# Kernel tuning notes

Measured on AMD Instinct MI355X. Metric: run time of the kernel, lower is better.

## Reference

```python
import jax, jax.numpy as jnp
import numpy as np

N_NODES = 100000
N_EDGES = 1600000
DIMS = [100, 200, 128, 128]
EPS = 1e-5


def setup_inputs() -> dict:
    key = jax.random.key(0)
    ks = jax.random.split(key, 32)
    inp = {
        "x": jax.random.normal(ks[0], (N_NODES, DIMS[0]), dtype=jnp.float32),
        "edge_row": jnp.sort(jax.random.randint(ks[1], (N_EDGES,), 0, N_NODES, dtype=jnp.int32)),
        "edge_col": jax.random.randint(ks[2], (N_EDGES,), 0, N_NODES, dtype=jnp.int32),
        "edge_val": jax.random.uniform(ks[3], (N_EDGES,), dtype=jnp.float32),
    }
    # GCwithself layer params: neighbor-agg linear W,b and self linear Ws,bs
    ki = 4
    for i in range(3):
        fi, fo = DIMS[i], DIMS[i + 1]
        s = 1.0 / np.sqrt(fi)
        inp[f"gc{i}_W"] = jax.random.uniform(ks[ki], (fi, fo), minval=-s, maxval=s); ki += 1
        inp[f"gc{i}_b"] = jnp.zeros((fo,), jnp.float32)
        inp[f"gc{i}_Ws"] = jax.random.uniform(ks[ki], (fi, fo), minval=-s, maxval=s); ki += 1
        inp[f"gc{i}_bs"] = jnp.zeros((fo,), jnp.float32)
    s = 1.0 / np.sqrt(128)
    inp["fc1_W"] = jax.random.uniform(ks[ki], (128, 128), minval=-s, maxval=s); ki += 1
    inp["fc1_b"] = jnp.zeros((128,), jnp.float32)
    inp["fc2a_W"] = jax.random.uniform(ks[ki], (128, 256), minval=-s, maxval=s); ki += 1
    inp["fc2a_b"] = jnp.zeros((256,), jnp.float32)
    inp["bn_g"] = jnp.ones((256,), jnp.float32)
    inp["bn_b"] = jnp.zeros((256,), jnp.float32)
    s2 = 1.0 / np.sqrt(256)
    inp["fc2b_W"] = jax.random.uniform(ks[ki], (256, 18), minval=-s2, maxval=s2); ki += 1
    inp["fc2b_b"] = jnp.zeros((18,), jnp.float32)
    return inp


def _gc_layer(x, row, col, val, W, b, Ws, bs):
    # spmm: (adj @ x) via gather + segment-sum, then linear + self-linear + ReLU
    agg = jax.ops.segment_sum(val[:, None] * x[col], row, num_segments=N_NODES)
    return jax.nn.relu(agg @ W + b + x @ Ws + bs)


def _batchnorm(h, g, b):
    mu = jnp.mean(h, axis=0)
    var = jnp.var(h, axis=0)
    return (h - mu) * jax.lax.rsqrt(var + EPS) * g + b


def reference(x, edge_row, edge_col, edge_val,
              gc0_W, gc0_b, gc0_Ws, gc0_bs,
              gc1_W, gc1_b, gc1_Ws, gc1_bs,
              gc2_W, gc2_b, gc2_Ws, gc2_bs,
              fc1_W, fc1_b, fc2a_W, fc2a_b, bn_g, bn_b, fc2b_W, fc2b_b):
    h = _gc_layer(x, edge_row, edge_col, edge_val, gc0_W, gc0_b, gc0_Ws, gc0_bs)
    h = _gc_layer(h, edge_row, edge_col, edge_val, gc1_W, gc1_b, gc1_Ws, gc1_bs)
    h = _gc_layer(h, edge_row, edge_col, edge_val, gc2_W, gc2_b, gc2_Ws, gc2_bs)
    h = jax.nn.relu(h @ fc1_W + fc1_b)
    h = _batchnorm(h @ fc2a_W + fc2a_b, bn_g, bn_b)
    h = jax.nn.relu(h)
    return h @ fc2b_W + fc2b_b
```

## Files before the change

kernel.cpp:

```cpp
#include <hip/hip_runtime.h>

#define N_NODES 100000
#define N_EDGES 1600000

typedef __attribute__((ext_vector_type(8))) short bf16x8;
typedef __attribute__((ext_vector_type(4))) float f32x4;

__device__ __forceinline__ unsigned short f2bf(float f) {
    unsigned u = __float_as_uint(f);
    u = (u + 0x7FFFu + ((u >> 16) & 1u)) >> 16;
    return (unsigned short)u;
}
__device__ __forceinline__ float bf2f(unsigned short h) {
    return __uint_as_float(((unsigned)h) << 16);
}
__device__ __forceinline__ float bflo(unsigned w) { return __uint_as_float(w << 16); }
__device__ __forceinline__ float bfhi(unsigned w) { return __uint_as_float(w & 0xFFFF0000u); }

__global__ void build_row_ptr(const int* __restrict__ row, int* __restrict__ rp) {
    int n = blockIdx.x * blockDim.x + threadIdx.x;
    if (n > N_NODES) return;
    int lo = 0, hi = N_EDGES;
    while (lo < hi) {
        int mid = (lo + hi) >> 1;
        if (row[mid] < n) lo = mid + 1; else hi = mid;
    }
    rp[n] = lo;
}

__global__ __launch_bounds__(256) void conv_x(const float* __restrict__ x,
                                              unsigned short* __restrict__ xb) {
    const int total = N_NODES * 104;
    for (int i = blockIdx.x * 256 + threadIdx.x; i < total; i += gridDim.x * 256) {
        int r = i / 104, c = i - r * 104;
        xb[i] = (c < 100) ? f2bf(x[(size_t)r * 100 + c]) : (unsigned short)0;
    }
}

__global__ __launch_bounds__(256) void prep_all(
    const float* __restrict__ gc0W, const float* __restrict__ gc0Ws,
    const float* __restrict__ gc1W, const float* __restrict__ gc1Ws,
    const float* __restrict__ gc2W, const float* __restrict__ gc2Ws,
    const float* __restrict__ f1W,  const float* __restrict__ f2aW,
    const float* __restrict__ f2bW,
    const float* __restrict__ gc0b, const float* __restrict__ gc0bs,
    const float* __restrict__ gc2b, const float* __restrict__ gc2bs,
    const float* __restrict__ gc1b, const float* __restrict__ gc1bs,
    unsigned short* __restrict__ Bt0, unsigned short* __restrict__ Bt1,
    unsigned short* __restrict__ Bt2, unsigned short* __restrict__ Btf1,
    unsigned short* __restrict__ Btf2a, unsigned short* __restrict__ Btf2b,
    float* __restrict__ bias0, float* __restrict__ bias2, float* __restrict__ bias1)
{
    int i = blockIdx.x * 256 + threadIdx.x;
    if (i < 44800) {
        int n = i / 224, k = i - n * 224; float v = 0.f;
        if (k < 104) { if (k < 100) v = gc0W[(size_t)k * 200 + n]; }
        else { int kr = k - 104; if (kr < 100) v = gc0Ws[(size_t)kr * 200 + n]; }
        Bt0[i] = f2bf(v); return;
    }
    i -= 44800;
    if (i < 57344) {
        int n = i / 224, k = i - n * 224; float v = 0.f;
        if (k < 200) v = (n < 128) ? gc1W[(size_t)k * 128 + n] : gc1Ws[(size_t)k * 128 + (n - 128)];
        Bt1[i] = f2bf(v); return;
    }
    i -= 57344;
    if (i < 32768) {
        int n = i / 256, k = i - n * 256; float v;
        if (k < 128) v = gc2W[(size_t)k * 128 + n];
        else         v = gc2Ws[(size_t)(k - 128) * 128 + n];
        Bt2[i] = f2bf(v); return;
    }
    i -= 32768;
    if (i < 16384) { int n = i >> 7, k = i & 127; Btf1[i] = f2bf(f1W[(size_t)k * 128 + n]); return; }
    i -= 16384;
    if (i < 32768) { int n = i >> 7, k = i & 127; Btf2a[i] = f2bf(f2aW[(size_t)k * 256 + n]); return; }
    i -= 32768;
    if (i < 4608) { int n = i >> 8, k = i & 255; Btf2b[i] = f2bf(f2bW[(size_t)k * 18 + n]); return; }
    i -= 4608;
    if (i < 200) { bias0[i] = gc0b[i] + gc0bs[i]; return; }
    i -= 200;
    if (i < 128) { bias2[i] = gc2b[i] + gc2bs[i]; return; }
    i -= 128;
    if (i < 128) { bias1[i] = gc1b[i] + gc1bs[i]; return; }
}

template<int FUSE>
__global__ __launch_bounds__(256) void spmm_v4(
    const unsigned short* __restrict__ xin, int ldin, int F,
    const int* __restrict__ rp, const int* __restrict__ col,
    const float* __restrict__ val, const float* __restrict__ b01,
    unsigned short* __restrict__ outp, int ldout)
{
    const int node = blockIdx.x * 16 + (threadIdx.x >> 4);
    const int l16 = threadIdx.x & 15;
    const int f8 = l16 * 8;
    const bool act = f8 < F;
    const int e0 = rp[node], e1 = rp[node + 1];
    const unsigned short* xf = xin + f8;

    float a[8];
#pragma unroll
    for (int k = 0; k < 8; k++) a[k] = 0.f;

    for (int e = e0; e < e1; e += 4) {
        int   cj[4]; float vj[4];
#pragma unroll
        for (int j = 0; j < 4; j++) {
            int ej = e + j;
            bool m = ej < e1;
            int es = m ? ej : e0;
            cj[j] = col[es];
            float vv = val[es];
            vj[j] = m ? vv : 0.f;
        }
        if (act) {
#pragma unroll
            for (int j = 0; j < 4; j++) {
                uint4 u = *(const uint4*)(xf + (size_t)cj[j] * ldin);
                float v = vj[j];
                a[0] += v * bflo(u.x); a[1] += v * bfhi(u.x);
                a[2] += v * bflo(u.y); a[3] += v * bfhi(u.y);
                a[4] += v * bflo(u.z); a[5] += v * bfhi(u.z);
                a[6] += v * bflo(u.w); a[7] += v * bfhi(u.w);
            }
        }
    }

    if (act) {
        if (FUSE) {
            uint4 uz = *(const uint4*)(xin + (size_t)node * ldin + 128 + f8);
            float z[8] = {bflo(uz.x), bfhi(uz.x), bflo(uz.y), bfhi(uz.y),
                          bflo(uz.z), bfhi(uz.z), bflo(uz.w), bfhi(uz.w)};
#pragma unroll
            for (int k = 0; k < 8; k++)
                a[k] = fmaxf(a[k] + z[k] + b01[f8 + k], 0.f);
        }
        uint4 pk;
        pk.x = ((unsigned)f2bf(a[1]) << 16) | (unsigned)f2bf(a[0]);
        pk.y = ((unsigned)f2bf(a[3]) << 16) | (unsigned)f2bf(a[2]);
        pk.z = ((unsigned)f2bf(a[5]) << 16) | (unsigned)f2bf(a[4]);
        pk.w = ((unsigned)f2bf(a[7]) << 16) | (unsigned)f2bf(a[6]);
        *(uint4*)(outp + (size_t)node * ldout + f8) = pk;
    }
}

__global__ __launch_bounds__(256, 2) void gemm_head(
    const unsigned short* __restrict__ agg0, const unsigned short* __restrict__ xb,
    const unsigned short* __restrict__ Bt0, const float* __restrict__ bias0,
    const unsigned short* __restrict__ Bt1,
    unsigned short* __restrict__ yz, int M)
{
    __shared__ __align__(16) unsigned short As[64][40];
    __shared__ __align__(16) unsigned short Bs[256][40];
    __shared__ __align__(16) unsigned short H[64][232];

    const int tid = threadIdx.x;
    const int rowBase = blockIdx.x * 64;
    const int wave = tid >> 6, lane = tid & 63;
    const int wc = wave * 64;
    const int lrow = lane & 15, lq = lane >> 4;

    {
        f32x4 acc[4][4] = {};
        for (int kk = 0; kk < 224; kk += 32) {
            {
                int row = tid >> 2;
                int kof = (tid & 3) * 8;
                int k0 = kk + kof;
                uint4 av = make_uint4(0, 0, 0, 0);
                int gr = rowBase + row;
                if (gr < M && k0 < 208) {
                    av = (k0 < 104) ? *(const uint4*)(agg0 + (size_t)gr * 104 + k0)
                                    : *(const uint4*)(xb   + (size_t)gr * 104 + (k0 - 104));
                }
                *(uint4*)&As[row][kof] = av;
            }
#pragma unroll
            for (int i = 0; i < 4; ++i) {
                int c = tid + 256 * i;
                int row = c >> 2;
                int kof = (c & 3) * 8;
                uint4 bv = make_uint4(0, 0, 0, 0);
                if (row < 200) bv = *(const uint4*)(Bt0 + (size_t)row * 224 + kk + kof);
                *(uint4*)&Bs[row][kof] = bv;
            }
            __syncthreads();
            bf16x8 af[4], bfr[4];
#pragma unroll
            for (int m = 0; m < 4; ++m) af[m] = *(const bf16x8*)&As[16 * m + lrow][lq * 8];
#pragma unroll
            for (int n = 0; n < 4; ++n) bfr[n] = *(const bf16x8*)&Bs[wc + 16 * n + lrow][lq * 8];
#pragma unroll
            for (int m = 0; m < 4; ++m)
#pragma unroll
                for (int n = 0; n < 4; ++n)
                    acc[m][n] = __builtin_amdgcn_mfma_f32_16x16x32_bf16(af[m], bfr[n], acc[m][n], 0, 0, 0);
            __syncthreads();
        }
#pragma unroll
        for (int n = 0; n < 4; ++n) {
            int colg = wc + 16 * n + lrow;
            if (colg >= 224) continue;
            float bb = (colg < 200) ? bias0[colg] : 0.f;
#pragma unroll
            for (int m = 0; m < 4; ++m)
#pragma unroll
                for (int r = 0; r < 4; ++r) {
                    int rowl = 16 * m + lq * 4 + r;
                    H[rowl][colg] = f2bf(fmaxf(acc[m][n][r] + bb, 0.f));
                }
        }
    }
    __syncthreads();

    {
        f32x4 acc[4][4] = {};
        for (int kk = 0; kk < 224; kk += 32) {
#pragma unroll
            for (int i = 0; i < 4; ++i) {
                int c = tid + 256 * i;
                int row = c >> 2;
                int kof = (c & 3) * 8;
                *(uint4*)&Bs[row][kof] = *(const uint4*)(Bt1 + (size_t)row * 224 + kk + kof);
            }
            __syncthreads();
            bf16x8 af[4], bfr[4];
#pragma unroll
            for (int m = 0; m < 4; ++m) af[m] = *(const bf16x8*)&H[16 * m + lrow][kk + lq * 8];
#pragma unroll
            for (int n = 0; n < 4; ++n) bfr[n] = *(const bf16x8*)&Bs[wc + 16 * n + lrow][lq * 8];
#pragma unroll
            for (int m = 0; m < 4; ++m)
#pragma unroll
                for (int n = 0; n < 4; ++n)
                    acc[m][n] = __builtin_amdgcn_mfma_f32_16x16x32_bf16(af[m], bfr[n], acc[m][n], 0, 0, 0);
            __syncthreads();
        }
#pragma unroll
        for (int n = 0; n < 4; ++n) {
            int colg = wc + 16 * n + lrow;
#pragma unroll
            for (int m = 0; m < 4; ++m)
#pragma unroll
                for (int r = 0; r < 4; ++r) {
                    int rowg = rowBase + 16 * m + lq * 4 + r;
                    if (rowg < M)
                        yz[(size_t)rowg * 256 + colg] = f2bf(acc[m][n][r]);
                }
        }
    }
}

template<int OUTBF, int APPLYBN>
__global__ __launch_bounds__(256) void gemm_mfma(
    const unsigned short* __restrict__ A0, const unsigned short* __restrict__ A1,
    int lda0, int lda1, int K0, int Ktot,
    const unsigned short* __restrict__ Bt, int ldk,
    const float* __restrict__ bias, void* __restrict__ Cv,
    int M, int N, int ldc, int relu, const float* __restrict__ stats)
{
    __shared__ __align__(16) unsigned short As[128][56];
    __shared__ __align__(16) unsigned short Bs[128][56];

    const int tid = threadIdx.x;
    const int rowBase = blockIdx.y * 128;
    const int colBase = blockIdx.x * 128;
    const int wave = tid >> 6, lane = tid & 63;
    const int wr = (wave >> 1) * 64, wc = (wave & 1) * 64;
    const int lrow = lane & 15, lq = lane >> 4;

    f32x4 acc[4][4] = {};

    for (int kk = 0; kk < ldk; kk += 32) {
#pragma unroll
        for (int i = 0; i < 2; ++i) {
            int c = tid + 256 * i;
            int row = c >> 2;
            int kof = (c & 3) * 8;
            int k0 = kk + kof;
            uint4 av = make_uint4(0, 0, 0, 0);
            int gr = rowBase + row;
            if (gr < M && k0 < Ktot) {
                const unsigned short* src; int krel;
                if (k0 < K0) { src = A0 + (size_t)gr * lda0; krel = k0; }
                else         { src = A1 + (size_t)gr * lda1; krel = k0 - K0; }
                av = *(const uint4*)(src + krel);
                if (APPLYBN) {
                    const float* sc = stats + 512 + k0;
                    const float* sh = stats + 768 + k0;
                    unsigned r[4] = {av.x, av.y, av.z, av.w};
#pragma unroll
                    for (int j = 0; j < 4; j++) {
                        float lo = bflo(r[j]) * sc[2 * j] + sh[2 * j];
                        float hi = bfhi(r[j]) * sc[2 * j + 1] + sh[2 * j + 1];
                        lo = fmaxf(lo, 0.f); hi = fmaxf(hi, 0.f);
                        r[j] = ((unsigned)f2bf(hi) << 16) | (unsigned)f2bf(lo);
                    }
                    av = make_uint4(r[0], r[1], r[2], r[3]);
                }
            }
            *(uint4*)&As[row][kof] = av;
            uint4 bv = make_uint4(0, 0, 0, 0);
            int n0 = colBase + row;
            if (n0 < N) bv = *(const uint4*)(Bt + (size_t)n0 * ldk + kk + kof);
            *(uint4*)&Bs[row][kof] = bv;
        }
        __syncthreads();

        bf16x8 af[4], bfr[4];
#pragma unroll
        for (int m = 0; m < 4; ++m) af[m] = *(const bf16x8*)&As[wr + 16 * m + lrow][lq * 8];
#pragma unroll
        for (int n = 0; n < 4; ++n) bfr[n] = *(const bf16x8*)&Bs[wc + 16 * n + lrow][lq * 8];
#pragma unroll
        for (int m = 0; m < 4; ++m)
#pragma unroll
            for (int n = 0; n < 4; ++n)
                acc[m][n] = __builtin_amdgcn_mfma_f32_16x16x32_bf16(af[m], bfr[n], acc[m][n], 0, 0, 0);
        __syncthreads();
    }

#pragma unroll
    for (int m = 0; m < 4; ++m) {
#pragma unroll
        for (int n = 0; n < 4; ++n) {
            int colg = colBase + wc + 16 * n + lrow;
            if (colg >= N) continue;
            float bb = bias ? bias[colg] : 0.f;
#pragma unroll
            for (int r = 0; r < 4; ++r) {
                int rowg = rowBase + wr + 16 * m + lq * 4 + r;
                if (rowg >= M) continue;
                float v = acc[m][n][r] + bb;
                if (relu) v = fmaxf(v, 0.f);
                if (OUTBF) ((unsigned short*)Cv)[(size_t)rowg * ldc + colg] = f2bf(v);
                else       ((float*)Cv)[(size_t)rowg * ldc + colg] = v;
            }
        }
    }
}

__global__ __launch_bounds__(256, 2) void gemm_tail(
    const unsigned short* __restrict__ agg2, const unsigned short* __restrict__ h1,
    const unsigned short* __restrict__ Bt2, const float* __restrict__ bias2,
    const unsigned short* __restrict__ Btf1, const float* __restrict__ fc1b,
    const unsigned short* __restrict__ Btf2a, const float* __restrict__ fc2ab,
    unsigned short* __restrict__ h4, float* __restrict__ stats, int M)
{
    __shared__ __align__(16) unsigned short As[128][56];
    __shared__ __align__(16) unsigned short Bs[256][56];
    __shared__ __align__(16) unsigned short H23[128][136];
    __shared__ float sred[512];

    const int tid = threadIdx.x;
    const int rowBase = blockIdx.x * 128;
    const int wave = tid >> 6, lane = tid & 63;
    const int wr = (wave >> 1) * 64, wc = (wave & 1) * 64;
    const int lrow = lane & 15, lq = lane >> 4;

    {
        f32x4 acc[4][4] = {};
        for (int kk = 0; kk < 256; kk += 32) {
#pragma unroll
            for (int i = 0; i < 2; ++i) {
                int c = tid + 256 * i;
                int row = c >> 2;
                int kof = (c & 3) * 8;
                int k0 = kk + kof;
                uint4 av = make_uint4(0, 0, 0, 0);
                int gr = rowBase + row;
                if (gr < M) {
                    av = (k0 < 128) ? *(const uint4*)(agg2 + (size_t)gr * 128 + k0)
                                    : *(const uint4*)(h1   + (size_t)gr * 128 + (k0 - 128));
                }
                *(uint4*)&As[row][kof] = av;
                *(uint4*)&Bs[row][kof] = *(const uint4*)(Bt2 + (size_t)row * 256 + k0);
            }
            __syncthreads();
            bf16x8 af[4], bfr[4];
#pragma unroll
            for (int m = 0; m < 4; ++m) af[m] = *(const bf16x8*)&As[wr + 16 * m + lrow][lq * 8];
#pragma unroll
            for (int n = 0; n < 4; ++n) bfr[n] = *(const bf16x8*)&Bs[wc + 16 * n + lrow][lq * 8];
#pragma unroll
            for (int m = 0; m < 4; ++m)
#pragma unroll
                for (int n = 0; n < 4; ++n)
                    acc[m][n] = __builtin_amdgcn_mfma_f32_16x16x32_bf16(af[m], bfr[n], acc[m][n], 0, 0, 0);
            __syncthreads();
        }
#pragma unroll
        for (int n = 0; n < 4; ++n) {
            int colg = wc + 16 * n + lrow;
            float bb = bias2[colg];
#pragma unroll
            for (int m = 0; m < 4; ++m)
#pragma unroll
                for (int r = 0; r < 4; ++r) {
                    int rowl = wr + 16 * m + lq * 4 + r;
                    H23[rowl][colg] = f2bf(fmaxf(acc[m][n][r] + bb, 0.f));
                }
        }
    }
    __syncthreads();

    {
        f32x4 acc[4][4] = {};
        for (int kk = 0; kk < 128; kk += 32) {
#pragma unroll
            for (int i = 0; i < 2; ++i) {
                int c = tid + 256 * i;
                int row = c >> 2;
                int kof = (c & 3) * 8;
                *(uint4*)&Bs[row][kof] = *(const uint4*)(Btf1 + (size_t)row * 128 + kk + kof);
            }
            __syncthreads();
            bf16x8 af[4], bfr[4];
#pragma unroll
            for (int m = 0; m < 4; ++m) af[m] = *(const bf16x8*)&H23[wr + 16 * m + lrow][kk + lq * 8];
#pragma unroll
            for (int n = 0; n < 4; ++n) bfr[n] = *(const bf16x8*)&Bs[wc + 16 * n + lrow][lq * 8];
#pragma unroll
            for (int m = 0; m < 4; ++m)
#pragma unroll
                for (int n = 0; n < 4; ++n)
                    acc[m][n] = __builtin_amdgcn_mfma_f32_16x16x32_bf16(af[m], bfr[n], acc[m][n], 0, 0, 0);
            __syncthreads();
        }
#pragma unroll
        for (int n = 0; n < 4; ++n) {
            int colg = wc + 16 * n + lrow;
            float bb = fc1b[colg];
#pragma unroll
            for (int m = 0; m < 4; ++m)
#pragma unroll
                for (int r = 0; r < 4; ++r) {
                    int rowl = wr + 16 * m + lq * 4 + r;
                    H23[rowl][colg] = f2bf(fmaxf(acc[m][n][r] + bb, 0.f));
                }
        }
    }
    __syncthreads();

    {
        f32x4 acc[4][8] = {};
        for (int kk = 0; kk < 128; kk += 32) {
#pragma unroll
            for (int i = 0; i < 4; ++i) {
                int c = tid + 256 * i;
                int row = c >> 2;
                int kof = (c & 3) * 8;
                *(uint4*)&Bs[row][kof] = *(const uint4*)(Btf2a + (size_t)row * 128 + kk + kof);
            }
            __syncthreads();
            bf16x8 af[4], bfr[8];
#pragma unroll
            for (int m = 0; m < 4; ++m) af[m] = *(const bf16x8*)&H23[wr + 16 * m + lrow][kk + lq * 8];
#pragma unroll
            for (int nh = 0; nh < 2; ++nh)
#pragma unroll
                for (int nm = 0; nm < 4; ++nm)
                    bfr[nh * 4 + nm] = *(const bf16x8*)&Bs[128 * nh + wc + 16 * nm + lrow][lq * 8];
#pragma unroll
            for (int m = 0; m < 4; ++m)
#pragma unroll
                for (int n = 0; n < 8; ++n)
                    acc[m][n] = __builtin_amdgcn_mfma_f32_16x16x32_bf16(af[m], bfr[n], acc[m][n], 0, 0, 0);
            __syncthreads();
        }

        for (int j = tid; j < 512; j += 256) sred[j] = 0.f;
        __syncthreads();
#pragma unroll
        for (int nh = 0; nh < 2; ++nh)
#pragma unroll
            for (int nm = 0; nm < 4; ++nm) {
                int colg = 128 * nh + wc + 16 * nm + lrow;
                float bb = fc2ab[colg];
                float s = 0.f, s2 = 0.f;
#pragma unroll
                for (int m = 0; m < 4; ++m)
#pragma unroll
                    for (int r = 0; r < 4; ++r) {
                        int rowg = rowBase + wr + 16 * m + lq * 4 + r;
                        if (rowg < M) {
                            float v = acc[m][nh * 4 + nm][r] + bb;
                            h4[(size_t)rowg * 256 + colg] = f2bf(v);
                            s += v; s2 += v * v;
                        }
                    }
                atomicAdd(&sred[colg], s);
                atomicAdd(&sred[256 + colg], s2);
            }
        __syncthreads();
        for (int j = tid; j < 512; j += 256) atomicAdd(&stats[j], sred[j]);
    }
}

__global__ void bn_finalize(float* __restrict__ stats,
                            const float* __restrict__ g,
                            const float* __restrict__ b) {
    int t = threadIdx.x;
    const float invN = 1.f / (float)N_NODES;
    float mu = stats[t] * invN;
    float var = stats[256 + t] * invN - mu * mu;
    float sc = g[t] * rsqrtf(var + 1e-5f);
    stats[512 + t] = sc;
    stats[768 + t] = b[t] - mu * sc;
}

extern "C" void kernel_launch(void* const* d_in, const int* in_sizes, int n_in,
                              void* d_out, int out_size, void* d_ws, size_t ws_size,
                              hipStream_t stream) {
    const float* x        = (const float*)d_in[0];
    const int*   edge_row = (const int*)  d_in[1];
    const int*   edge_col = (const int*)  d_in[2];
    const float* edge_val = (const float*)d_in[3];
    const float* gc0_W  = (const float*)d_in[4];
    const float* gc0_b  = (const float*)d_in[5];
    const float* gc0_Ws = (const float*)d_in[6];
    const float* gc0_bs = (const float*)d_in[7];
    const float* gc1_W  = (const float*)d_in[8];
    const float* gc1_b  = (const float*)d_in[9];
    const float* gc1_Ws = (const float*)d_in[10];
    const float* gc1_bs = (const float*)d_in[11];
    const float* gc2_W  = (const float*)d_in[12];
    const float* gc2_b  = (const float*)d_in[13];
    const float* gc2_Ws = (const float*)d_in[14];
    const float* gc2_bs = (const float*)d_in[15];
    const float* fc1_W  = (const float*)d_in[16];
    const float* fc1_b  = (const float*)d_in[17];
    const float* fc2a_W = (const float*)d_in[18];
    const float* fc2a_b = (const float*)d_in[19];
    const float* bn_g   = (const float*)d_in[20];
    const float* bn_b   = (const float*)d_in[21];
    const float* fc2b_W = (const float*)d_in[22];
    const float* fc2b_b = (const float*)d_in[23];
    float* out = (float*)d_out;

    char* ws = (char*)d_ws;
    int*   rowptr = (int*)ws;
    float* stats  = (float*)(ws + 512 * 1024);
    size_t o = 520 * 1024;
    unsigned short* Bt0   = (unsigned short*)(ws + o); o += 200 * 224 * 2;
    unsigned short* Bt1   = (unsigned short*)(ws + o); o += 256 * 224 * 2;
    unsigned short* Bt2   = (unsigned short*)(ws + o); o += 128 * 256 * 2;
    unsigned short* Btf1  = (unsigned short*)(ws + o); o += 128 * 128 * 2;
    unsigned short* Btf2a = (unsigned short*)(ws + o); o += 256 * 128 * 2;
    unsigned short* Btf2b = (unsigned short*)(ws + o); o += 18 * 256 * 2;
    float* bias0 = (float*)(ws + o); o += 200 * 4;
    float* bias2 = (float*)(ws + o); o += 128 * 4;
    float* bias1 = (float*)(ws + o); o += 128 * 4;
    const size_t SLOT = 52u * 1024 * 1024;
    char* S1 = ws + 1 * 1024 * 1024;
    char* S2 = S1 + SLOT;
    char* S3 = S2 + SLOT;

    unsigned short* xb   = (unsigned short*)S1;
    unsigned short* agg0 = (unsigned short*)S2;
    unsigned short* yz   = (unsigned short*)S3;
    unsigned short* h1   = (unsigned short*)S1;
    unsigned short* agg2 = (unsigned short*)S2;
    unsigned short* h4   = (unsigned short*)S3;

    build_row_ptr<<<392, 256, 0, stream>>>(edge_row, rowptr);
    conv_x<<<2048, 256, 0, stream>>>(x, xb);
    prep_all<<<(189128 + 255) / 256, 256, 0, stream>>>(
        gc0_W, gc0_Ws, gc1_W, gc1_Ws, gc2_W, gc2_Ws, fc1_W, fc2a_W, fc2b_W,
        gc0_b, gc0_bs, gc2_b, gc2_bs, gc1_b, gc1_bs,
        Bt0, Bt1, Bt2, Btf1, Btf2a, Btf2b, bias0, bias2, bias1);
    hipMemsetAsync(stats, 0, 512 * sizeof(float), stream);

    const int spmmGrid = N_NODES / 16;

    spmm_v4<0><<<spmmGrid, 256, 0, stream>>>(xb, 104, 104, rowptr, edge_col, edge_val,
                                             nullptr, agg0, 104);
    gemm_head<<<(N_NODES + 63) / 64, 256, 0, stream>>>(agg0, xb, Bt0, bias0, Bt1, yz, N_NODES);
    spmm_v4<1><<<spmmGrid, 256, 0, stream>>>(yz, 256, 128, rowptr, edge_col, edge_val,
                                             bias1, h1, 128);
    spmm_v4<0><<<spmmGrid, 256, 0, stream>>>(h1, 128, 128, rowptr, edge_col, edge_val,
                                             nullptr, agg2, 128);
    gemm_tail<<<(N_NODES + 127) / 128, 256, 0, stream>>>(
        agg2, h1, Bt2, bias2, Btf1, fc1_b, Btf2a, fc2a_b, h4, stats, N_NODES);
    bn_finalize<<<1, 256, 0, stream>>>(stats, bn_g, bn_b);
    {
        dim3 g(1, (N_NODES + 127) / 128);
        gemm_mfma<0, 1><<<g, 256, 0, stream>>>(h4, h4, 256, 256, 256, 256, Btf2b, 256,
                                               fc2b_b, out, N_NODES, 18, 18, 0, stats);
    }
}
```

Baseline: 537.9 us.

## Load MFMA fragments directly from global memory, shrink tail tiles, specialize fc2b

The dense GEMM kernels (head, tail, and final fc2b) stop staging A and B tiles through shared memory with barriers. Each lane now loads its MFMA fragments straight from global memory, and shared memory is kept only for the intermediate activations. gemm_tail moves to 64-row tiles with occupancy hint 4. The generic gemm_mfma call for the 18-column output is replaced by a dedicated kernel that gives each wave 32 rows and skips the unused columns. This removes LDS traffic and synchronization and raises occupancy, at the cost of redundant global/L2 loads of weights across waves and less coalesced fragment reads.

```diff
diff --git a/kernel.cpp b/kernel.cpp
--- a/kernel.cpp
+++ b/kernel.cpp
@@ -16,6 +16,10 @@
 }
 __device__ __forceinline__ float bflo(unsigned w) { return __uint_as_float(w << 16); }
 __device__ __forceinline__ float bfhi(unsigned w) { return __uint_as_float(w & 0xFFFF0000u); }
+
+__device__ __forceinline__ bf16x8 ld_frag(const unsigned short* p) {
+    return *(const bf16x8*)p;
+}
 
 __global__ void build_row_ptr(const int* __restrict__ row, int* __restrict__ rp) {
     int n = blockIdx.x * blockDim.x + threadIdx.x;
@@ -145,62 +149,51 @@
     }
 }
 
-__global__ __launch_bounds__(256, 2) void gemm_head(
+__global__ __launch_bounds__(256, 4) void gemm_head(
     const unsigned short* __restrict__ agg0, const unsigned short* __restrict__ xb,
     const unsigned short* __restrict__ Bt0, const float* __restrict__ bias0,
     const unsigned short* __restrict__ Bt1,
     unsigned short* __restrict__ yz, int M)
 {
-    __shared__ __align__(16) unsigned short As[64][40];
-    __shared__ __align__(16) unsigned short Bs[256][40];
     __shared__ __align__(16) unsigned short H[64][232];
 
     const int tid = threadIdx.x;
     const int rowBase = blockIdx.x * 64;
     const int wave = tid >> 6, lane = tid & 63;
-    const int wc = wave * 64;
+    const int cb = wave * 64;
     const int lrow = lane & 15, lq = lane >> 4;
+    const int kq = lq * 8;
 
     {
         f32x4 acc[4][4] = {};
         for (int kk = 0; kk < 224; kk += 32) {
-            {
-                int row = tid >> 2;
-                int kof = (tid & 3) * 8;
-                int k0 = kk + kof;
-                uint4 av = make_uint4(0, 0, 0, 0);
-                int gr = rowBase + row;
-                if (gr < M && k0 < 208) {
-                    av = (k0 < 104) ? *(const uint4*)(agg0 + (size_t)gr * 104 + k0)
-                                    : *(const uint4*)(xb   + (size_t)gr * 104 + (k0 - 104));
-                }
-                *(uint4*)&As[row][kof] = av;
+            int k0 = kk + kq;
+            bf16x8 af[4], bfr[4];
+#pragma unroll
+            for (int m = 0; m < 4; ++m) {
+                int gr = rowBase + 16 * m + lrow;
+                bf16x8 t = {};
+                if (gr < M && k0 < 208)
+                    t = (k0 < 104) ? ld_frag(agg0 + (size_t)gr * 104 + k0)
+                                   : ld_frag(xb   + (size_t)gr * 104 + (k0 - 104));
+                af[m] = t;
             }
 #pragma unroll
-            for (int i = 0; i < 4; ++i) {
-                int c = tid + 256 * i;
-                int row = c >> 2;
-                int kof = (c & 3) * 8;
-                uint4 bv = make_uint4(0, 0, 0, 0);
-                if (row < 200) bv = *(const uint4*)(Bt0 + (size_t)row * 224 + kk + kof);
-                *(uint4*)&Bs[row][kof] = bv;
+            for (int n = 0; n < 4; ++n) {
+                int nr = cb + 16 * n + lrow;
+                bf16x8 t = {};
+                if (nr < 200) t = ld_frag(Bt0 + (size_t)nr * 224 + k0);
+                bfr[n] = t;
             }
-            __syncthreads();
-            bf16x8 af[4], bfr[4];
-#pragma unroll
-            for (int m = 0; m < 4; ++m) af[m] = *(const bf16x8*)&As[16 * m + lrow][lq * 8];
-#pragma unroll
-            for (int n = 0; n < 4; ++n) bfr[n] = *(const bf16x8*)&Bs[wc + 16 * n + lrow][lq * 8];
 #pragma unroll
             for (int m = 0; m < 4; ++m)
 #pragma unroll
                 for (int n = 0; n < 4; ++n)
                     acc[m][n] = __builtin_amdgcn_mfma_f32_16x16x32_bf16(af[m], bfr[n], acc[m][n], 0, 0, 0);
-            __syncthreads();
         }
 #pragma unroll
         for (int n = 0; n < 4; ++n) {
-            int colg = wc + 16 * n + lrow;
+            int colg = cb + 16 * n + lrow;
             if (colg >= 224) continue;
             float bb = (colg < 200) ? bias0[colg] : 0.f;
 #pragma unroll
@@ -217,29 +210,22 @@
     {
         f32x4 acc[4][4] = {};
         for (int kk = 0; kk < 224; kk += 32) {
-#pragma unroll
-            for (int i = 0; i < 4; ++i) {
-                int c = tid + 256 * i;
-                int row = c >> 2;
-                int kof = (c & 3) * 8;
-                *(uint4*)&Bs[row][kof] = *(const uint4*)(Bt1 + (size_t)row * 224 + kk + kof);
-            }
-            __syncthreads();
+            int k0 = kk + kq;
             bf16x8 af[4], bfr[4];
 #pragma unroll
-            for (int m = 0; m < 4; ++m) af[m] = *(const bf16x8*)&H[16 * m + lrow][kk + lq * 8];
-#pragma unroll
-            for (int n = 0; n < 4; ++n) bfr[n] = *(const bf16x8*)&Bs[wc + 16 * n + lrow][lq * 8];
+            for (int m = 0; m < 4; ++m) af[m] = *(const bf16x8*)&H[16 * m + lrow][k0];
+#pragma unroll
+            for (int n = 0; n < 4; ++n)
+                bfr[n] = ld_frag(Bt1 + (size_t)(cb + 16 * n + lrow) * 224 + k0);
 #pragma unroll
             for (int m = 0; m < 4; ++m)
 #pragma unroll
                 for (int n = 0; n < 4; ++n)
                     acc[m][n] = __builtin_amdgcn_mfma_f32_16x16x32_bf16(af[m], bfr[n], acc[m][n], 0, 0, 0);
-            __syncthreads();
         }
 #pragma unroll
         for (int n = 0; n < 4; ++n) {
-            int colg = wc + 16 * n + lrow;
+            int colg = cb + 16 * n + lrow;
 #pragma unroll
             for (int m = 0; m < 4; ++m)
 #pragma unroll
@@ -252,247 +238,133 @@
     }
 }
 
-template<int OUTBF, int APPLYBN>
-__global__ __launch_bounds__(256) void gemm_mfma(
-    const unsigned short* __restrict__ A0, const unsigned short* __restrict__ A1,
-    int lda0, int lda1, int K0, int Ktot,
-    const unsigned short* __restrict__ Bt, int ldk,
-    const float* __restrict__ bias, void* __restrict__ Cv,
-    int M, int N, int ldc, int relu, const float* __restrict__ stats)
-{
-    __shared__ __align__(16) unsigned short As[128][56];
-    __shared__ __align__(16) unsigned short Bs[128][56];
-
-    const int tid = threadIdx.x;
-    const int rowBase = blockIdx.y * 128;
-    const int colBase = blockIdx.x * 128;
-    const int wave = tid >> 6, lane = tid & 63;
-    const int wr = (wave >> 1) * 64, wc = (wave & 1) * 64;
-    const int lrow = lane & 15, lq = lane >> 4;
-
-    f32x4 acc[4][4] = {};
-
-    for (int kk = 0; kk < ldk; kk += 32) {
-#pragma unroll
-        for (int i = 0; i < 2; ++i) {
-            int c = tid + 256 * i;
-            int row = c >> 2;
-            int kof = (c & 3) * 8;
-            int k0 = kk + kof;
-            uint4 av = make_uint4(0, 0, 0, 0);
-            int gr = rowBase + row;
-            if (gr < M && k0 < Ktot) {
-                const unsigned short* src; int krel;
-                if (k0 < K0) { src = A0 + (size_t)gr * lda0; krel = k0; }
-                else         { src = A1 + (size_t)gr * lda1; krel = k0 - K0; }
-                av = *(const uint4*)(src + krel);
-                if (APPLYBN) {
-                    const float* sc = stats + 512 + k0;
-                    const float* sh = stats + 768 + k0;
-                    unsigned r[4] = {av.x, av.y, av.z, av.w};
-#pragma unroll
-                    for (int j = 0; j < 4; j++) {
-                        float lo = bflo(r[j]) * sc[2 * j] + sh[2 * j];
-                        float hi = bfhi(r[j]) * sc[2 * j + 1] + sh[2 * j + 1];
-                        lo = fmaxf(lo, 0.f); hi = fmaxf(hi, 0.f);
-                        r[j] = ((unsigned)f2bf(hi) << 16) | (unsigned)f2bf(lo);
-                    }
-                    av = make_uint4(r[0], r[1], r[2], r[3]);
-                }
-            }
-            *(uint4*)&As[row][kof] = av;
-            uint4 bv = make_uint4(0, 0, 0, 0);
-            int n0 = colBase + row;
-            if (n0 < N) bv = *(const uint4*)(Bt + (size_t)n0 * ldk + kk + kof);
-            *(uint4*)&Bs[row][kof] = bv;
-        }
-        __syncthreads();
-
-        bf16x8 af[4], bfr[4];
-#pragma unroll
-        for (int m = 0; m < 4; ++m) af[m] = *(const bf16x8*)&As[wr + 16 * m + lrow][lq * 8];
-#pragma unroll
-        for (int n = 0; n < 4; ++n) bfr[n] = *(const bf16x8*)&Bs[wc + 16 * n + lrow][lq * 8];
-#pragma unroll
-        for (int m = 0; m < 4; ++m)
-#pragma unroll
-            for (int n = 0; n < 4; ++n)
-                acc[m][n] = __builtin_amdgcn_mfma_f32_16x16x32_bf16(af[m], bfr[n], acc[m][n], 0, 0, 0);
-        __syncthreads();
-    }
-
-#pragma unroll
-    for (int m = 0; m < 4; ++m) {
-#pragma unroll
-        for (int n = 0; n < 4; ++n) {
-            int colg = colBase + wc + 16 * n + lrow;
-            if (colg >= N) continue;
-            float bb = bias ? bias[colg] : 0.f;
-#pragma unroll
-            for (int r = 0; r < 4; ++r) {
-                int rowg = rowBase + wr + 16 * m + lq * 4 + r;
-                if (rowg >= M) continue;
-                float v = acc[m][n][r] + bb;
-                if (relu) v = fmaxf(v, 0.f);
-                if (OUTBF) ((unsigned short*)Cv)[(size_t)rowg * ldc + colg] = f2bf(v);
-                else       ((float*)Cv)[(size_t)rowg * ldc + colg] = v;
-            }
-        }
-    }
-}
-
-__global__ __launch_bounds__(256, 2) void gemm_tail(
+__global__ __launch_bounds__(256, 4) void gemm_tail(
     const unsigned short* __restrict__ agg2, const unsigned short* __restrict__ h1,
     const unsigned short* __restrict__ Bt2, const float* __restrict__ bias2,
     const unsigned short* __restrict__ Btf1, const float* __restrict__ fc1b,
     const unsigned short* __restrict__ Btf2a, const float* __restrict__ fc2ab,
     unsigned short* __restrict__ h4, float* __restrict__ stats, int M)
 {
-    __shared__ __align__(16) unsigned short As[128][56];
-    __shared__ __align__(16) unsigned short Bs[256][56];
-    __shared__ __align__(16) unsigned short H23[128][136];
+    __shared__ __align__(16) unsigned short H[64][136];
     __shared__ float sred[512];
 
     const int tid = threadIdx.x;
-    const int rowBase = blockIdx.x * 128;
+    const int rowBase = blockIdx.x * 64;
     const int wave = tid >> 6, lane = tid & 63;
-    const int wr = (wave >> 1) * 64, wc = (wave & 1) * 64;
     const int lrow = lane & 15, lq = lane >> 4;
+    const int kq = lq * 8;
 
     {
+        const int cb = wave * 32;
+        f32x4 acc[4][2] = {};
+        for (int kk = 0; kk < 256; kk += 32) {
+            int k0 = kk + kq;
+            const unsigned short* Asrc = (kk < 128) ? agg2 : h1;
+            int krel = (kk < 128) ? k0 : k0 - 128;
+            bf16x8 af[4], bfr[2];
+#pragma unroll
+            for (int m = 0; m < 4; ++m) {
+                int gr = rowBase + 16 * m + lrow;
+                bf16x8 t = {};
+                if (gr < M) t = ld_frag(Asrc + (size_t)gr * 128 + krel);
+                af[m] = t;
+            }
+#pragma unroll
+            for (int n = 0; n < 2; ++n)
+                bfr[n] = ld_frag(Bt2 + (size_t)(cb + 16 * n + lrow) * 256 + k0);
+#pragma unroll
+            for (int m = 0; m < 4; ++m)
+#pragma unroll
+                for (int n = 0; n < 2; ++n)
+                    acc[m][n] = __builtin_amdgcn_mfma_f32_16x16x32_bf16(af[m], bfr[n], acc[m][n], 0, 0, 0);
+        }
+#pragma unroll
+        for (int n = 0; n < 2; ++n) {
+            int colg = cb + 16 * n + lrow;
+            float bb = bias2[colg];
+#pragma unroll
+            for (int m = 0; m < 4; ++m)
+#pragma unroll
+                for (int r = 0; r < 4; ++r) {
+                    int rowl = 16 * m + lq * 4 + r;
+                    H[rowl][colg] = f2bf(fmaxf(acc[m][n][r] + bb, 0.f));
+                }
+        }
+    }
+    __syncthreads();
+
+    {
+        const int cb = wave * 32;
+        f32x4 acc[4][2] = {};
+        for (int kk = 0; kk < 128; kk += 32) {
+            int k0 = kk + kq;
+            bf16x8 af[4], bfr[2];
+#pragma unroll
+            for (int m = 0; m < 4; ++m) af[m] = *(const bf16x8*)&H[16 * m + lrow][k0];
+#pragma unroll
+            for (int n = 0; n < 2; ++n)
+                bfr[n] = ld_frag(Btf1 + (size_t)(cb + 16 * n + lrow) * 128 + k0);
+#pragma unroll
+            for (int m = 0; m < 4; ++m)
+#pragma unroll
+                for (int n = 0; n < 2; ++n)
+                    acc[m][n] = __builtin_amdgcn_mfma_f32_16x16x32_bf16(af[m], bfr[n], acc[m][n], 0, 0, 0);
+        }
+        __syncthreads();
+#pragma unroll
+        for (int n = 0; n < 2; ++n) {
+            int colg = cb + 16 * n + lrow;
+            float bb = fc1b[colg];
+#pragma unroll
+            for (int m = 0; m < 4; ++m)
+#pragma unroll
+                for (int r = 0; r < 4; ++r) {
+                    int rowl = 16 * m + lq * 4 + r;
+                    H[rowl][colg] = f2bf(fmaxf(acc[m][n][r] + bb, 0.f));
+                }
+        }
+    }
+    __syncthreads();
+
+    {
+        const int cb = wave * 64;
         f32x4 acc[4][4] = {};
-        for (int kk = 0; kk < 256; kk += 32) {
-#pragma unroll
-            for (int i = 0; i < 2; ++i) {
-                int c = tid + 256 * i;
-                int row = c >> 2;
-                int kof = (c & 3) * 8;
-                int k0 = kk + kof;
-                uint4 av = make_uint4(0, 0, 0, 0);
-                int gr = rowBase + row;
-                if (gr < M) {
-                    av = (k0 < 128) ? *(const uint4*)(agg2 + (size_t)gr * 128 + k0)
-                                    : *(const uint4*)(h1   + (size_t)gr * 128 + (k0 - 128));
-                }
-                *(uint4*)&As[row][kof] = av;
-                *(uint4*)&Bs[row][kof] = *(const uint4*)(Bt2 + (size_t)row * 256 + k0);
-            }
-            __syncthreads();
+        for (int kk = 0; kk < 128; kk += 32) {
+            int k0 = kk + kq;
             bf16x8 af[4], bfr[4];
 #pragma unroll
-            for (int m = 0; m < 4; ++m) af[m] = *(const bf16x8*)&As[wr + 16 * m + lrow][lq * 8];
-#pragma unroll
-            for (int n = 0; n < 4; ++n) bfr[n] = *(const bf16x8*)&Bs[wc + 16 * n + lrow][lq * 8];
+            for (int m = 0; m < 4; ++m) af[m] = *(const bf16x8*)&H[16 * m + lrow][k0];
+#pragma unroll
+            for (int n = 0; n < 4; ++n)
+                bfr[n] = ld_frag(Btf2a + (size_t)(cb + 16 * n + lrow) * 128 + k0);
 #pragma unroll
             for (int m = 0; m < 4; ++m)
 #pragma unroll
                 for (int n = 0; n < 4; ++n)
                     acc[m][n] = __builtin_amdgcn_mfma_f32_16x16x32_bf16(af[m], bfr[n], acc[m][n], 0, 0, 0);
-            __syncthreads();
-        }
-#pragma unroll
-        for (int n = 0; n < 4; ++n) {
-            int colg = wc + 16 * n + lrow;
-            float bb = bias2[colg];
-#pragma unroll
-            for (int m = 0; m < 4; ++m)
-#pragma unroll
-                for (int r = 0; r < 4; ++r) {
-                    int rowl = wr + 16 * m + lq * 4 + r;
-                    H23[rowl][colg] = f2bf(fmaxf(acc[m][n][r] + bb, 0.f));
-                }
-        }
-    }
-    __syncthreads();
-
-    {
-        f32x4 acc[4][4] = {};
-        for (int kk = 0; kk < 128; kk += 32) {
-#pragma unroll
-            for (int i = 0; i < 2; ++i) {
-                int c = tid + 256 * i;
-                int row = c >> 2;
-                int kof = (c & 3) * 8;
-                *(uint4*)&Bs[row][kof] = *(const uint4*)(Btf1 + (size_t)row * 128 + kk + kof);
-            }
-            __syncthreads();
-            bf16x8 af[4], bfr[4];
-#pragma unroll
-            for (int m = 0; m < 4; ++m) af[m] = *(const bf16x8*)&H23[wr + 16 * m + lrow][kk + lq * 8];
-#pragma unroll
-            for (int n = 0; n < 4; ++n) bfr[n] = *(const bf16x8*)&Bs[wc + 16 * n + lrow][lq * 8];
-#pragma unroll
-            for (int m = 0; m < 4; ++m)
-#pragma unroll
-                for (int n = 0; n < 4; ++n)
-                    acc[m][n] = __builtin_amdgcn_mfma_f32_16x16x32_bf16(af[m], bfr[n], acc[m][n], 0, 0, 0);
-            __syncthreads();
-        }
-#pragma unroll
-        for (int n = 0; n < 4; ++n) {
-            int colg = wc + 16 * n + lrow;
-            float bb = fc1b[colg];
-#pragma unroll
-            for (int m = 0; m < 4; ++m)
-#pragma unroll
-                for (int r = 0; r < 4; ++r) {
-                    int rowl = wr + 16 * m + lq * 4 + r;
-                    H23[rowl][colg] = f2bf(fmaxf(acc[m][n][r] + bb, 0.f));
-                }
-        }
-    }
-    __syncthreads();
-
-    {
-        f32x4 acc[4][8] = {};
-        for (int kk = 0; kk < 128; kk += 32) {
-#pragma unroll
-            for (int i = 0; i < 4; ++i) {
-                int c = tid + 256 * i;
-                int row = c >> 2;
-                int kof = (c & 3) * 8;
-                *(uint4*)&Bs[row][kof] = *(const uint4*)(Btf2a + (size_t)row * 128 + kk + kof);
-            }
-            __syncthreads();
-            bf16x8 af[4], bfr[8];
-#pragma unroll
-            for (int m = 0; m < 4; ++m) af[m] = *(const bf16x8*)&H23[wr + 16 * m + lrow][kk + lq * 8];
-#pragma unroll
-            for (int nh = 0; nh < 2; ++nh)
-#pragma unroll
-                for (int nm = 0; nm < 4; ++nm)
-                    bfr[nh * 4 + nm] = *(const bf16x8*)&Bs[128 * nh + wc + 16 * nm + lrow][lq * 8];
-#pragma unroll
-            for (int m = 0; m < 4; ++m)
-#pragma unroll
-                for (int n = 0; n < 8; ++n)
-                    acc[m][n] = __builtin_amdgcn_mfma_f32_16x16x32_bf16(af[m], bfr[n], acc[m][n], 0, 0, 0);
-            __syncthreads();
         }
 
         for (int j = tid; j < 512; j += 256) sred[j] = 0.f;
         __syncthreads();
 #pragma unroll
-        for (int nh = 0; nh < 2; ++nh)
-#pragma unroll
-            for (int nm = 0; nm < 4; ++nm) {
-                int colg = 128 * nh + wc + 16 * nm + lrow;
-                float bb = fc2ab[colg];
-                float s = 0.f, s2 = 0.f;
-#pragma unroll
-                for (int m = 0; m < 4; ++m)
-#pragma unroll
-                    for (int r = 0; r < 4; ++r) {
-                        int rowg = rowBase + wr + 16 * m + lq * 4 + r;
-                        if (rowg < M) {
-                            float v = acc[m][nh * 4 + nm][r] + bb;
-                            h4[(size_t)rowg * 256 + colg] = f2bf(v);
-                            s += v; s2 += v * v;
-                        }
+        for (int n = 0; n < 4; ++n) {
+            int colg = cb + 16 * n + lrow;
+            float bb = fc2ab[colg];
+            float s = 0.f, s2 = 0.f;
+#pragma unroll
+            for (int m = 0; m < 4; ++m)
+#pragma unroll
+                for (int r = 0; r < 4; ++r) {
+                    int rowg = rowBase + 16 * m + lq * 4 + r;
+                    if (rowg < M) {
+                        float v = acc[m][n][r] + bb;
+                        h4[(size_t)rowg * 256 + colg] = f2bf(v);
+                        s += v; s2 += v * v;
                     }
-                atomicAdd(&sred[colg], s);
-                atomicAdd(&sred[256 + colg], s2);
-            }
+                }
+            atomicAdd(&sred[colg], s);
+            atomicAdd(&sred[256 + colg], s2);
+        }
         __syncthreads();
         for (int j = tid; j < 512; j += 256) atomicAdd(&stats[j], sred[j]);
     }
@@ -508,6 +380,67 @@
     float sc = g[t] * rsqrtf(var + 1e-5f);
     stats[512 + t] = sc;
     stats[768 + t] = b[t] - mu * sc;
+}
+
+__global__ __launch_bounds__(256, 4) void fc2b_kernel(
+    const unsigned short* __restrict__ h4, const unsigned short* __restrict__ Btf2b,
+    const float* __restrict__ bias, const float* __restrict__ stats,
+    float* __restrict__ out, int M)
+{
+    const int tid = threadIdx.x;
+    const int wave = tid >> 6, lane = tid & 63;
+    const int lrow = lane & 15, lq = lane >> 4;
+    const int kq = lq * 8;
+    const int rowBase = blockIdx.x * 128 + wave * 32;
+
+    f32x4 acc[2][2] = {};
+    for (int kk = 0; kk < 256; kk += 32) {
+        int k0 = kk + kq;
+        const float* sc = stats + 512 + k0;
+        const float* sh = stats + 768 + k0;
+        bf16x8 af[2], bfr[2];
+#pragma unroll
+        for (int m = 0; m < 2; ++m) {
+            int gr = rowBase + 16 * m + lrow;
+            uint4 u = make_uint4(0, 0, 0, 0);
+            if (gr < M) u = *(const uint4*)(h4 + (size_t)gr * 256 + k0);
+            unsigned w[4] = {u.x, u.y, u.z, u.w};
+#pragma unroll
+            for (int j = 0; j < 4; j++) {
+                float lo = fmaxf(bflo(w[j]) * sc[2 * j] + sh[2 * j], 0.f);
+                float hi = fmaxf(bfhi(w[j]) * sc[2 * j + 1] + sh[2 * j + 1], 0.f);
+                w[j] = ((unsigned)f2bf(hi) << 16) | (unsigned)f2bf(lo);
+            }
+            uint4 packed = make_uint4(w[0], w[1], w[2], w[3]);
+            af[m] = *(const bf16x8*)&packed;
+        }
+#pragma unroll
+        for (int n = 0; n < 2; ++n) {
+            int nr = 16 * n + lrow;
+            bf16x8 t = {};
+            if (nr < 18) t = ld_frag(Btf2b + (size_t)nr * 256 + k0);
+            bfr[n] = t;
+        }
+#pragma unroll
+        for (int m = 0; m < 2; ++m)
+#pragma unroll
+            for (int n = 0; n < 2; ++n)
+                acc[m][n] = __builtin_amdgcn_mfma_f32_16x16x32_bf16(af[m], bfr[n], acc[m][n], 0, 0, 0);
+    }
+#pragma unroll
+    for (int n = 0; n < 2; ++n) {
+        int colg = 16 * n + lrow;
+        if (colg >= 18) continue;
+        float bb = bias[colg];
+#pragma unroll
+        for (int m = 0; m < 2; ++m)
+#pragma unroll
+            for (int r = 0; r < 4; ++r) {
+                int rowg = rowBase + 16 * m + lq * 4 + r;
+                if (rowg < M)
+                    out[(size_t)rowg * 18 + colg] = acc[m][n][r] + bb;
+            }
+    }
 }
 
 extern "C" void kernel_launch(void* const* d_in, const int* in_sizes, int n_in,
@@ -573,20 +506,18 @@
     hipMemsetAsync(stats, 0, 512 * sizeof(float), stream);
 
     const int spmmGrid = N_NODES / 16;
+    const int tile64 = (N_NODES + 63) / 64;
 
     spmm_v4<0><<<spmmGrid, 256, 0, stream>>>(xb, 104, 104, rowptr, edge_col, edge_val,
                                              nullptr, agg0, 104);
-    gemm_head<<<(N_NODES + 63) / 64, 256, 0, stream>>>(agg0, xb, Bt0, bias0, Bt1, yz, N_NODES);
+    gemm_head<<<tile64, 256, 0, stream>>>(agg0, xb, Bt0, bias0, Bt1, yz, N_NODES);
     spmm_v4<1><<<spmmGrid, 256, 0, stream>>>(yz, 256, 128, rowptr, edge_col, edge_val,
                                              bias1, h1, 128);
     spmm_v4<0><<<spmmGrid, 256, 0, stream>>>(h1, 128, 128, rowptr, edge_col, edge_val,
                                              nullptr, agg2, 128);
-    gemm_tail<<<(N_NODES + 127) / 128, 256, 0, stream>>>(
+    gemm_tail<<<tile64, 256, 0, stream>>>(
         agg2, h1, Bt2, bias2, Btf1, fc1_b, Btf2a, fc2a_b, h4, stats, N_NODES);
     bn_finalize<<<1, 256, 0, stream>>>(stats, bn_g, bn_b);
-    {
-        dim3 g(1, (N_NODES + 127) / 128);
-        gemm_mfma<0, 1><<<g, 256, 0, stream>>>(h4, h4, 256, 256, 256, 256, Btf2b, 256,
-                                               fc2b_b, out, N_NODES, 18, 18, 0, stats);
-    }
-}
+    fc2b_kernel<<<(N_NODES + 127) / 128, 256, 0, stream>>>(
+        h4, Btf2b, fc2b_b, stats, out, N_NODES);
+}
```

New measurement: 544.8 us. Within noise of the previous version (+1.3%).
